# Kernel tuning notes

Measured on AMD Instinct MI355X. Metric: run time of the kernel, lower is better.

## Reference

```python
import jax, jax.numpy as jnp
import numpy as np

N, DQ, T, H1 = 131072, 256, 4, 512

def setup_inputs() -> dict:
    key = jax.random.key(0)
    k_q, k_w0, k_b0, k_w1, k_z = jax.random.split(key, 5)
    return {
        "q": jax.random.normal(k_q, (N, DQ), dtype=jnp.float32),
        "Z": jax.random.randint(k_z, (N,), 0, T, dtype=jnp.int32),
        "W0": jax.random.normal(k_w0, (T, DQ, H1), dtype=jnp.float32) * (1.0 / np.sqrt(DQ)),
        "b0": jax.random.normal(k_b0, (T, H1), dtype=jnp.float32) * 0.01,
        "W1": jax.random.normal(k_w1, (T, H1), dtype=jnp.float32) * (1.0 / np.sqrt(H1)),
        "b1": jnp.zeros((), dtype=jnp.float32),
    }

def reference(q, Z, W0, b0, W1, b1):
    # Dense grouped-GEMM over all T types (T is small), then select per-atom
    # type result. Avoids materializing the per-atom [N, dq, h1] gathered
    # weight tensor that tf.gather would create.
    h_all = jnp.einsum('nd,tdh->nth', q, W0)              # [N, T, H1]
    h = jnp.take_along_axis(h_all, Z[:, None, None].astype(jnp.int32), axis=1)[:, 0, :]  # [N, H1]
    h = jnp.tanh(h + b0[Z])                               # hidden activations
    F = jnp.einsum('nh,nh->n', h, W1[Z]) + b1             # [N]
    return F
```

## Files before the change

kernel.cpp:

```cpp
#include <hip/hip_runtime.h>
#include <hip/hip_bf16.h>

#define N_ATOMS 131072
#define DQ 256
#define H1 512
#define NTYPES 4
#define TILE_M 64
#define NPAD (N_ATOMS + NTYPES * TILE_M)
#define BLOCKS_PER_TYPE 64
#define ROWPAD 65

typedef __bf16 bf16x8 __attribute__((ext_vector_type(8)));
typedef float f32x16 __attribute__((ext_vector_type(16)));

__device__ __forceinline__ unsigned int pack2(float a, float b) {
  unsigned int ua = __builtin_bit_cast(unsigned int, a);
  unsigned int ub = __builtin_bit_cast(unsigned int, b);
  ua += 0x7fffu + ((ua >> 16) & 1u);
  ub += 0x7fffu + ((ub >> 16) & 1u);
  return __builtin_amdgcn_perm(ub, ua, 0x07060302);
}
__device__ __forceinline__ unsigned short f2bf(float f) {
  unsigned int u = __builtin_bit_cast(unsigned int, f);
  u += 0x7fffu + ((u >> 16) & 1u);
  return (unsigned short)(u >> 16);
}
__device__ __forceinline__ float fast_tanh(float x) {
  float e = __expf(2.0f * x);
  return 1.0f - 2.0f * __builtin_amdgcn_rcpf(e + 1.0f);
}
template <int CTRL>
__device__ __forceinline__ float dpp_add(float s) {
  int v = __builtin_amdgcn_mov_dpp(__builtin_bit_cast(int, s), CTRL, 0xF, 0xF, true);
  return s + __builtin_bit_cast(float, v);
}

__global__ __launch_bounds__(256) void prep_kernel(
    const float* __restrict__ W0, const int* __restrict__ Z,
    unsigned short* __restrict__ W0s, int* __restrict__ perm,
    int* __restrict__ blockcounts)
{
  __shared__ int lc[NTYPES];
  __shared__ __align__(16) unsigned short S[64][72];
  const int b = blockIdx.x, tid = threadIdx.x;
  const int gid = b * 256 + tid;

  for (int i = gid; i < NPAD; i += 512 * 256) perm[i] = -1;
  if (tid < NTYPES) lc[tid] = 0;
  __syncthreads();
  atomicAdd(&lc[Z[gid]], 1);

  if (b < 128) {
    const int nb = b & 7, kb = (b >> 3) & 3, t = b >> 5;
    const int kl = tid >> 4, nl = (tid & 15) * 4;
#pragma unroll
    for (int r = 0; r < 4; ++r) {
      const int k = r * 16 + kl;
      const float4 v = *(const float4*)&W0[((size_t)(t * DQ + kb * 64 + k)) * H1 + nb * 64 + nl];
      S[nl + 0][k] = f2bf(v.x);
      S[nl + 1][k] = f2bf(v.y);
      S[nl + 2][k] = f2bf(v.z);
      S[nl + 3][k] = f2bf(v.w);
    }
    __syncthreads();
#pragma unroll
    for (int r = 0; r < 2; ++r) {
      const int c = r * 256 + tid;
      const int n = c & 63, kg2l = c >> 6;
      const uint4 v = *(const uint4*)&S[n][kg2l * 8];
      ((uint4*)W0s)[(size_t)(t * 32 + kb * 8 + kg2l) * H1 + nb * 64 + n] = v;
    }
  }
  __syncthreads();
  if (tid < NTYPES) blockcounts[b * NTYPES + tid] = lc[tid];
}

__global__ __launch_bounds__(256) void scan_kernel(
    const int* __restrict__ blockcounts, int* __restrict__ padded_off,
    int* __restrict__ cursors)
{
  __shared__ int sums[NTYPES];
  const int tid = threadIdx.x;
  if (tid < NTYPES) sums[tid] = 0;
  __syncthreads();
  const int t = tid & 3;
  int acc = 0;
  for (int b = tid >> 2; b < 512; b += 64) acc += blockcounts[b * 4 + t];
  atomicAdd(&sums[t], acc);
  __syncthreads();
  if (tid == 0) {
    int off = 0;
#pragma unroll
    for (int i = 0; i < NTYPES; ++i) {
      padded_off[i] = off;
      cursors[i] = off;
      off += (sums[i] + TILE_M - 1) & ~(TILE_M - 1);
    }
    padded_off[NTYPES] = off;
  }
}

__global__ __launch_bounds__(256) void scatter_kernel(
    const int* __restrict__ Z, int* __restrict__ cursors, int* __restrict__ perm)
{
  __shared__ int lc[NTYPES], lbase[NTYPES];
  const int tid = threadIdx.x;
  const int gid = blockIdx.x * 256 + tid;
  if (tid < NTYPES) lc[tid] = 0;
  __syncthreads();
  const int t  = Z[gid];
  const int my = atomicAdd(&lc[t], 1);
  __syncthreads();
  if (tid < NTYPES) lbase[tid] = lc[tid] ? atomicAdd(&cursors[tid], lc[tid]) : 0;
  __syncthreads();
  perm[lbase[t] + my] = gid;
}

__global__ __launch_bounds__(512, 2) void gemm_kernel(
    const float* __restrict__ q, const int* __restrict__ perm,
    const int* __restrict__ padded_off, const unsigned short* __restrict__ W0s,
    const float* __restrict__ b0, const float* __restrict__ W1,
    const float* __restrict__ b1p, float* __restrict__ out)
{
  __shared__ __align__(16) unsigned short A[2][32 * ROWPAD * 8];
  __shared__ float Fws[8][64];

  const int tid = threadIdx.x;
  const int w = tid >> 6, l = tid & 63;
  const int half = l >> 5, ln = l & 31;

  const int t = blockIdx.x >> 6;
  const int bslot = blockIdx.x & 63;
  const int seg0 = padded_off[t];
  const int ntiles = (padded_off[t + 1] - seg0) >> 6;
  if (bslot >= ntiles) return;

  const int colbase = w * 64;

  float b0v[2], w1v[2];
#pragma unroll
  for (int nt = 0; nt < 2; ++nt) {
    const int c = colbase + nt * 32 + ln;
    b0v[nt] = b0[t * H1 + c];
    w1v[nt] = W1[t * H1 + c];
  }
  const float b1 = b1p[0];

  const unsigned short* Bt = W0s + (size_t)t * (DQ * H1);
  bf16x8 Bf[16][2];
#pragma unroll
  for (int ks = 0; ks < 16; ++ks) {
    const int kg2 = ks * 2 + half;
#pragma unroll
    for (int nt = 0; nt < 2; ++nt)
      Bf[ks][nt] = *(const bf16x8*)(Bt + ((size_t)kg2 * H1 + colbase + nt * 32 + ln) * 8);
  }

  int j = bslot;
  int row0 = seg0 + (j << 6);
#pragma unroll
  for (int i = 0; i < 8; ++i) {
    int a = perm[row0 + w * 8 + i];
    if (a < 0) a = 0;
    const float4 v = *(const float4*)(q + (size_t)a * DQ + l * 4);
    uint2 u;
    u.x = pack2(v.x, v.y);
    u.y = pack2(v.z, v.w);
    *(uint2*)&A[0][((l >> 1) * ROWPAD + w * 8 + i) * 8 + (l & 1) * 4] = u;
  }
  __syncthreads();
  int p = 0;

  for (;;) {
    const int jn = j + BLOCKS_PER_TYPE;
    const bool have_next = jn < ntiles;
    const int rbase = have_next ? seg0 + (jn << 6) : row0;

    float4 ld[8];
#pragma unroll
    for (int i = 0; i < 8; ++i) {
      int a = perm[rbase + w * 8 + i];
      if (a < 0) a = 0;
      ld[i] = *(const float4*)(q + (size_t)a * DQ + l * 4);
    }
    __builtin_amdgcn_sched_barrier(0);

    const unsigned short* Acur = A[p];
    f32x16 acc[2][2];
#pragma unroll
    for (int mt = 0; mt < 2; ++mt)
#pragma unroll
      for (int nt = 0; nt < 2; ++nt) acc[mt][nt] = (f32x16)0.0f;

#pragma unroll
    for (int ks = 0; ks < 16; ++ks) {
      const int kg2 = ks * 2 + half;
      const bf16x8 a0 = *(const bf16x8*)&Acur[(kg2 * ROWPAD + ln) * 8];
      const bf16x8 a1 = *(const bf16x8*)&Acur[(kg2 * ROWPAD + 32 + ln) * 8];
      acc[0][0] = __builtin_amdgcn_mfma_f32_32x32x16_bf16(a0, Bf[ks][0], acc[0][0], 0, 0, 0);
      acc[1][0] = __builtin_amdgcn_mfma_f32_32x32x16_bf16(a1, Bf[ks][0], acc[1][0], 0, 0, 0);
      acc[0][1] = __builtin_amdgcn_mfma_f32_32x32x16_bf16(a0, Bf[ks][1], acc[0][1], 0, 0, 0);
      acc[1][1] = __builtin_amdgcn_mfma_f32_32x32x16_bf16(a1, Bf[ks][1], acc[1][1], 0, 0, 0);
    }

#pragma unroll
    for (int mt = 0; mt < 2; ++mt) {
#pragma unroll
      for (int r = 0; r < 16; ++r) {
        float s = w1v[0] * fast_tanh(acc[mt][0][r] + b0v[0])
                + w1v[1] * fast_tanh(acc[mt][1][r] + b0v[1]);
        s = dpp_add<0xB1>(s);
        s = dpp_add<0x4E>(s);
        s += __shfl_xor(s, 4);
        s = dpp_add<0x128>(s);
        s += __shfl_xor(s, 16);
        if (ln == 0)
          Fws[w][mt * 32 + (r & 3) + 8 * (r >> 2) + 4 * half] = s;
      }
    }
    __syncthreads();

    if (tid < TILE_M) {
      const int atom = perm[row0 + tid];
      if (atom >= 0) {
        float f = b1;
#pragma unroll
        for (int ww = 0; ww < 8; ++ww) f += Fws[ww][tid];
        out[atom] = f;
      }
    }

#pragma unroll
    for (int i = 0; i < 8; ++i) {
      uint2 u;
      u.x = pack2(ld[i].x, ld[i].y);
      u.y = pack2(ld[i].z, ld[i].w);
      *(uint2*)&A[1 - p][((l >> 1) * ROWPAD + w * 8 + i) * 8 + (l & 1) * 4] = u;
    }

    if (!have_next) break;
    __syncthreads();
    p ^= 1;
    j = jn;
    row0 = rbase;
  }
}

extern "C" void kernel_launch(void* const* d_in, const int* in_sizes, int n_in,
                              void* d_out, int out_size, void* d_ws, size_t ws_size,
                              hipStream_t stream) {
  const float* q  = (const float*)d_in[0];
  const int*   Z  = (const int*)d_in[1];
  const float* W0 = (const float*)d_in[2];
  const float* b0 = (const float*)d_in[3];
  const float* W1 = (const float*)d_in[4];
  const float* b1 = (const float*)d_in[5];
  float* out = (float*)d_out;

  char* ws = (char*)d_ws;
  int* blockcounts = (int*)(ws);
  int* padded_off  = (int*)(ws + 8192);
  int* cursors     = (int*)(ws + 8192 + 32);
  int* perm        = (int*)(ws + 8192 + 64);
  unsigned short* W0s = (unsigned short*)(ws + 8192 + 64 + (size_t)NPAD * 4);

  hipLaunchKernelGGL(prep_kernel,    dim3(512), dim3(256), 0, stream, W0, Z, W0s, perm, blockcounts);
  hipLaunchKernelGGL(scan_kernel,    dim3(1),   dim3(256), 0, stream, blockcounts, padded_off, cursors);
  hipLaunchKernelGGL(scatter_kernel, dim3(512), dim3(256), 0, stream, Z, cursors, perm);
  hipLaunchKernelGGL(gemm_kernel,    dim3(NTYPES * BLOCKS_PER_TYPE), dim3(512), 0, stream,
                     q, perm, padded_off, W0s, b0, W1, b1, out);
}
```

Before: 292.6 us.

## Split q gather into separate kernel writing pre-tiled bf16 buffer

Adds a gather kernel that permutes q rows by type and converts them to bf16 in MFMA-fragment layout in global memory. The GEMM kernel then reads A fragments straight from that buffer instead of staging through double-buffered LDS. This drops the in-kernel gather, the LDS traffic and one barrier per tile, and Fws is double-buffered by parity to remove the remaining hazard. In exchange it adds a kernel launch and an extra global write and read of a bf16 copy of q (about 64 MB), and the GEMM now waits on global-memory latency with no explicit prefetch.

```diff
diff --git a/kernel.cpp b/kernel.cpp
--- a/kernel.cpp
+++ b/kernel.cpp
@@ -7,8 +7,7 @@
 #define NTYPES 4
 #define TILE_M 64
 #define NPAD (N_ATOMS + NTYPES * TILE_M)
-#define BLOCKS_PER_TYPE 64
-#define ROWPAD 65
+#define BLOCK_SLOTS 64
 
 typedef __bf16 bf16x8 __attribute__((ext_vector_type(8)));
 typedef float f32x16 __attribute__((ext_vector_type(16)));
@@ -116,21 +115,56 @@
   perm[lbase[t] + my] = gid;
 }
 
+__device__ __forceinline__ void gather_row(const float* __restrict__ q,
+    const int* __restrict__ perm, unsigned short* __restrict__ qs,
+    int r, int l)
+{
+  const int atom = perm[r];
+  uint2 u;
+  if (atom >= 0) {
+    const float4 v = *(const float4*)(q + (size_t)atom * DQ + l * 4);
+    u.x = pack2(v.x, v.y);
+    u.y = pack2(v.z, v.w);
+  } else {
+    u.x = 0u; u.y = 0u;
+  }
+  unsigned short* tb = qs + (size_t)(r >> 6) * (32 * 64 * 8);
+  *(uint2*)&tb[(((l >> 1) * 64) + (r & 63)) * 8 + (l & 1) * 4] = u;
+}
+
+__global__ __launch_bounds__(256) void gather_kernel(
+    const float* __restrict__ q, const int* __restrict__ perm,
+    const int* __restrict__ padded_off, unsigned short* __restrict__ qs)
+{
+  const int wid = (blockIdx.x * 256 + threadIdx.x) >> 6;
+  const int l = threadIdx.x & 63;
+  const int total = padded_off[NTYPES];
+  const int r0 = wid * 32;
+  if (r0 + 32 <= total) {
+#pragma unroll 4
+    for (int i = 0; i < 32; ++i) gather_row(q, perm, qs, r0 + i, l);
+  } else {
+    for (int i = 0; i < 32; ++i) {
+      const int r = r0 + i;
+      if (r < total) gather_row(q, perm, qs, r, l);
+    }
+  }
+}
+
 __global__ __launch_bounds__(512, 2) void gemm_kernel(
-    const float* __restrict__ q, const int* __restrict__ perm,
+    const unsigned short* __restrict__ qs, const int* __restrict__ perm,
     const int* __restrict__ padded_off, const unsigned short* __restrict__ W0s,
     const float* __restrict__ b0, const float* __restrict__ W1,
     const float* __restrict__ b1p, float* __restrict__ out)
 {
-  __shared__ __align__(16) unsigned short A[2][32 * ROWPAD * 8];
-  __shared__ float Fws[8][64];
+  __shared__ float Fws[2][8][64];
 
   const int tid = threadIdx.x;
   const int w = tid >> 6, l = tid & 63;
   const int half = l >> 5, ln = l & 31;
 
   const int t = blockIdx.x >> 6;
-  const int bslot = blockIdx.x & 63;
+  const int bslot = blockIdx.x & (BLOCK_SLOTS - 1);
   const int seg0 = padded_off[t];
   const int ntiles = (padded_off[t + 1] - seg0) >> 6;
   if (bslot >= ntiles) return;
@@ -156,36 +190,11 @@
       Bf[ks][nt] = *(const bf16x8*)(Bt + ((size_t)kg2 * H1 + colbase + nt * 32 + ln) * 8);
   }
 
-  int j = bslot;
-  int row0 = seg0 + (j << 6);
-#pragma unroll
-  for (int i = 0; i < 8; ++i) {
-    int a = perm[row0 + w * 8 + i];
-    if (a < 0) a = 0;
-    const float4 v = *(const float4*)(q + (size_t)a * DQ + l * 4);
-    uint2 u;
-    u.x = pack2(v.x, v.y);
-    u.y = pack2(v.z, v.w);
-    *(uint2*)&A[0][((l >> 1) * ROWPAD + w * 8 + i) * 8 + (l & 1) * 4] = u;
-  }
-  __syncthreads();
-  int p = 0;
-
-  for (;;) {
-    const int jn = j + BLOCKS_PER_TYPE;
-    const bool have_next = jn < ntiles;
-    const int rbase = have_next ? seg0 + (jn << 6) : row0;
-
-    float4 ld[8];
-#pragma unroll
-    for (int i = 0; i < 8; ++i) {
-      int a = perm[rbase + w * 8 + i];
-      if (a < 0) a = 0;
-      ld[i] = *(const float4*)(q + (size_t)a * DQ + l * 4);
-    }
-    __builtin_amdgcn_sched_barrier(0);
-
-    const unsigned short* Acur = A[p];
+  int parity = 0;
+  for (int j = bslot; j < ntiles; j += BLOCK_SLOTS, parity ^= 1) {
+    const int row0 = seg0 + (j << 6);
+    const unsigned short* At = qs + (size_t)row0 * 256;
+
     f32x16 acc[2][2];
 #pragma unroll
     for (int mt = 0; mt < 2; ++mt)
@@ -193,14 +202,22 @@
       for (int nt = 0; nt < 2; ++nt) acc[mt][nt] = (f32x16)0.0f;
 
 #pragma unroll
-    for (int ks = 0; ks < 16; ++ks) {
-      const int kg2 = ks * 2 + half;
-      const bf16x8 a0 = *(const bf16x8*)&Acur[(kg2 * ROWPAD + ln) * 8];
-      const bf16x8 a1 = *(const bf16x8*)&Acur[(kg2 * ROWPAD + 32 + ln) * 8];
-      acc[0][0] = __builtin_amdgcn_mfma_f32_32x32x16_bf16(a0, Bf[ks][0], acc[0][0], 0, 0, 0);
-      acc[1][0] = __builtin_amdgcn_mfma_f32_32x32x16_bf16(a1, Bf[ks][0], acc[1][0], 0, 0, 0);
-      acc[0][1] = __builtin_amdgcn_mfma_f32_32x32x16_bf16(a0, Bf[ks][1], acc[0][1], 0, 0, 0);
-      acc[1][1] = __builtin_amdgcn_mfma_f32_32x32x16_bf16(a1, Bf[ks][1], acc[1][1], 0, 0, 0);
+    for (int g = 0; g < 4; ++g) {
+      bf16x8 Ab[4][2];
+#pragma unroll
+      for (int ks = 0; ks < 4; ++ks) {
+        const int kg2 = (g * 4 + ks) * 2 + half;
+        Ab[ks][0] = *(const bf16x8*)&At[(kg2 * 64 + ln) * 8];
+        Ab[ks][1] = *(const bf16x8*)&At[(kg2 * 64 + 32 + ln) * 8];
+      }
+#pragma unroll
+      for (int ks = 0; ks < 4; ++ks) {
+        const int k = g * 4 + ks;
+        acc[0][0] = __builtin_amdgcn_mfma_f32_32x32x16_bf16(Ab[ks][0], Bf[k][0], acc[0][0], 0, 0, 0);
+        acc[1][0] = __builtin_amdgcn_mfma_f32_32x32x16_bf16(Ab[ks][1], Bf[k][0], acc[1][0], 0, 0, 0);
+        acc[0][1] = __builtin_amdgcn_mfma_f32_32x32x16_bf16(Ab[ks][0], Bf[k][1], acc[0][1], 0, 0, 0);
+        acc[1][1] = __builtin_amdgcn_mfma_f32_32x32x16_bf16(Ab[ks][1], Bf[k][1], acc[1][1], 0, 0, 0);
+      }
     }
 
 #pragma unroll
@@ -215,7 +232,7 @@
         s = dpp_add<0x128>(s);
         s += __shfl_xor(s, 16);
         if (ln == 0)
-          Fws[w][mt * 32 + (r & 3) + 8 * (r >> 2) + 4 * half] = s;
+          Fws[parity][w][mt * 32 + (r & 3) + 8 * (r >> 2) + 4 * half] = s;
       }
     }
     __syncthreads();
@@ -225,24 +242,10 @@
       if (atom >= 0) {
         float f = b1;
 #pragma unroll
-        for (int ww = 0; ww < 8; ++ww) f += Fws[ww][tid];
+        for (int ww = 0; ww < 8; ++ww) f += Fws[parity][ww][tid];
         out[atom] = f;
       }
     }
-
-#pragma unroll
-    for (int i = 0; i < 8; ++i) {
-      uint2 u;
-      u.x = pack2(ld[i].x, ld[i].y);
-      u.y = pack2(ld[i].z, ld[i].w);
-      *(uint2*)&A[1 - p][((l >> 1) * ROWPAD + w * 8 + i) * 8 + (l & 1) * 4] = u;
-    }
-
-    if (!have_next) break;
-    __syncthreads();
-    p ^= 1;
-    j = jn;
-    row0 = rbase;
   }
 }
 
@@ -263,10 +266,13 @@
   int* cursors     = (int*)(ws + 8192 + 32);
   int* perm        = (int*)(ws + 8192 + 64);
   unsigned short* W0s = (unsigned short*)(ws + 8192 + 64 + (size_t)NPAD * 4);
-
-  hipLaunchKernelGGL(prep_kernel,    dim3(512), dim3(256), 0, stream, W0, Z, W0s, perm, blockcounts);
-  hipLaunchKernelGGL(scan_kernel,    dim3(1),   dim3(256), 0, stream, blockcounts, padded_off, cursors);
-  hipLaunchKernelGGL(scatter_kernel, dim3(512), dim3(256), 0, stream, Z, cursors, perm);
-  hipLaunchKernelGGL(gemm_kernel,    dim3(NTYPES * BLOCKS_PER_TYPE), dim3(512), 0, stream,
-                     q, perm, padded_off, W0s, b0, W1, b1, out);
-}
+  unsigned short* qs  = (unsigned short*)(ws + 8192 + 64 + (size_t)NPAD * 4
+                                          + (size_t)NTYPES * DQ * H1 * 2);
+
+  hipLaunchKernelGGL(prep_kernel,    dim3(512),  dim3(256), 0, stream, W0, Z, W0s, perm, blockcounts);
+  hipLaunchKernelGGL(scan_kernel,    dim3(1),    dim3(256), 0, stream, blockcounts, padded_off, cursors);
+  hipLaunchKernelGGL(scatter_kernel, dim3(512),  dim3(256), 0, stream, Z, cursors, perm);
+  hipLaunchKernelGGL(gather_kernel,  dim3(1026), dim3(256), 0, stream, q, perm, padded_off, qs);
+  hipLaunchKernelGGL(gemm_kernel,    dim3(NTYPES * BLOCK_SLOTS), dim3(512), 0, stream,
+                     qs, perm, padded_off, W0s, b0, W1, b1, out);
+}
```

New measurement: 373.5 us. +27.7%, slower.
